# Kernel tuning notes

Measured on AMD Instinct MI355X. Metric: run time of the kernel, lower is better.

## Reference

```python
import jax, jax.numpy as jnp
import numpy as np

REL_CONTEXT = 0.2  # default forward arg

def setup_inputs() -> dict:
    key = jax.random.key(0)
    ks = jax.random.split(key, 8)
    B, M, D = 4096, 2, 2048
    return {
        "x": jax.random.normal(ks[0], (B, M, D), jnp.float32),
        "sub_type_ids": jax.random.randint(ks[1], (B, M), 0, M),
        "modal_weights": jnp.ones((M,), jnp.float32),
        "emb_table": jax.random.normal(ks[2], (M, D), jnp.float32),
        "Wt": jax.random.normal(ks[3], (D, D), jnp.float32) * (1.0 / np.sqrt(D)),
        "bt": jax.random.normal(ks[4], (D,), jnp.float32) * 0.01,
        "Wrc": jax.random.normal(ks[5], (1, D), jnp.float32) * (1.0 / np.sqrt(D)),
        "brc": jax.random.normal(ks[6], (1,), jnp.float32) * 0.01,
    }

def reference(x, sub_type_ids, modal_weights, emb_table, Wt, bt, Wrc, brc):
    B = x.shape[0]
    D = emb_table.shape[1]
    x = x.reshape(B, -1, D)  # [B, M, D]
    # relational gate: Linear(D->1) on a constant vector filled with 0.2 -> scalar
    rc = jnp.full((D,), REL_CONTEXT, dtype=x.dtype)
    zeta = jax.nn.sigmoid(rc @ Wrc.T + brc)  # [1]
    sub = emb_table[sub_type_ids]  # [B, M, D] embedding lookup
    # fused: per-modality Linear + ReLU (replaces the B*M python loop)
    t = jax.nn.relu(jnp.einsum('bmd,ed->bme', x + sub, Wt) + bt)  # [B, M, D]
    h = modal_weights[None, :, None] * t * zeta[0]
    # dropout is identity in eval mode; final ReLU as in the original
    return jax.nn.relu(h)
```

## Files before the change

### kernel.cpp

```cpp
#include <hip/hip_runtime.h>
#include <hip/hip_bf16.h>
#include <math.h>

#define MROWS 8192
#define KDIM  2048
#define NDIM  2048

#define BM 256
#define BN 256
#define BK 64
#define NT (KDIM / BK)

typedef short  v8s __attribute__((ext_vector_type(8)));
typedef float  v4f __attribute__((ext_vector_type(4)));

#define A_OFF   0ull
#define W_OFF   ((unsigned long long)MROWS * KDIM * 2ull)
#define MWZ_OFF (W_OFF + (unsigned long long)NDIM * KDIM * 2ull)

__device__ inline unsigned short f2bf(float f) {
    __hip_bfloat16 h = __float2bfloat16(f);
    return *reinterpret_cast<unsigned short*>(&h);
}

__global__ __launch_bounds__(256) void prep_kernel(
    const float* __restrict__ x, const int* __restrict__ ids,
    const float* __restrict__ mw, const float* __restrict__ emb,
    const float* __restrict__ Wrc, const float* __restrict__ brc,
    const float* __restrict__ Wt,
    unsigned short* __restrict__ Abf, unsigned short* __restrict__ Wbf,
    float* __restrict__ mwz)
{
    const int tid = threadIdx.x;

    if (blockIdx.x == 0) {
        __shared__ float red[256];
        float s = 0.f;
        for (int d = tid; d < KDIM; d += 256) s += Wrc[d];
        red[tid] = s;
        __syncthreads();
        for (int off = 128; off > 0; off >>= 1) {
            if (tid < off) red[tid] += red[tid + off];
            __syncthreads();
        }
        if (tid == 0) {
            float zeta = 1.0f / (1.0f + expf(-(0.2f * red[0] + brc[0])));
            mwz[0] = mw[0] * zeta;
            mwz[1] = mw[1] * zeta;
        }
    }

    const int groupsA = MROWS * KDIM / 8;
    for (int g = blockIdx.x * 256 + tid; g < groupsA; g += gridDim.x * 256) {
        const int row = g >> 8;
        const int off = (g & 255) << 3;
        const int st  = ids[row];
        const float4* xp = (const float4*)(x   + (size_t)row * KDIM + off);
        const float4* ep = (const float4*)(emb + (size_t)st  * KDIM + off);
        float4 x0 = xp[0], x1 = xp[1];
        float4 e0 = ep[0], e1 = ep[1];
        v8s o;
        o[0] = (short)f2bf(x0.x + e0.x);
        o[1] = (short)f2bf(x0.y + e0.y);
        o[2] = (short)f2bf(x0.z + e0.z);
        o[3] = (short)f2bf(x0.w + e0.w);
        o[4] = (short)f2bf(x1.x + e1.x);
        o[5] = (short)f2bf(x1.y + e1.y);
        o[6] = (short)f2bf(x1.z + e1.z);
        o[7] = (short)f2bf(x1.w + e1.w);
        *(v8s*)(Abf + (size_t)g * 8) = o;
    }

    const int groupsW = NDIM * KDIM / 8;
    for (int g = blockIdx.x * 256 + tid; g < groupsW; g += gridDim.x * 256) {
        const float4* wp = (const float4*)(Wt + (size_t)g * 8);
        float4 w0 = wp[0], w1 = wp[1];
        v8s o;
        o[0] = (short)f2bf(w0.x); o[1] = (short)f2bf(w0.y);
        o[2] = (short)f2bf(w0.z); o[3] = (short)f2bf(w0.w);
        o[4] = (short)f2bf(w1.x); o[5] = (short)f2bf(w1.y);
        o[6] = (short)f2bf(w1.z); o[7] = (short)f2bf(w1.w);
        *(v8s*)(Wbf + (size_t)g * 8) = o;
    }
}


#define SBAR()   __builtin_amdgcn_s_barrier()
#define LGKM0()  asm volatile("s_waitcnt lgkmcnt(0)" ::: "memory")
#define VMCNT(n) asm volatile("s_waitcnt vmcnt(" #n ")" ::: "memory")

template<int P>
__device__ __forceinline__ void mfma_phase(v4f (&acc)[8][4],
                                           const v8s (&b)[4][2],
                                           const v8s (&a)[2][2])
{
    __builtin_amdgcn_s_setprio(1);
    #pragma unroll
    for (int j = 0; j < 4; ++j) {
        acc[2*P  ][j] = __builtin_amdgcn_mfma_f32_16x16x32_bf16(b[j][0], a[0][0], acc[2*P  ][j], 0, 0, 0);
        acc[2*P+1][j] = __builtin_amdgcn_mfma_f32_16x16x32_bf16(b[j][0], a[1][0], acc[2*P+1][j], 0, 0, 0);
    }
    #pragma unroll
    for (int j = 0; j < 4; ++j) {
        acc[2*P  ][j] = __builtin_amdgcn_mfma_f32_16x16x32_bf16(b[j][1], a[0][1], acc[2*P  ][j], 0, 0, 0);
        acc[2*P+1][j] = __builtin_amdgcn_mfma_f32_16x16x32_bf16(b[j][1], a[1][1], acc[2*P+1][j], 0, 0, 0);
    }
    __builtin_amdgcn_s_setprio(0);
}

#define KTILE2(CA, CB, NA, NB, T)                                         \
  {                                                                       \
    if ((T) + 1 < NT) {                                                   \
      stage(NB, gB, (T) + 1, 0); stage(NB, gB, (T) + 1, 1);               \
      stage(NB, gB, (T) + 1, 2); stage(NB, gB, (T) + 1, 3);               \
      stage(NA, gA, (T) + 1, 0); stage(NA, gA, (T) + 1, 1);               \
      stage(NA, gA, (T) + 1, 2); stage(NA, gA, (T) + 1, 3);               \
    }                                                                     \
    v8s a[2][2], b[4][2];                                                 \
    b[0][0] = rdB(CB, 0, 0); b[0][1] = rdB(CB, 0, 1);                     \
    b[1][0] = rdB(CB, 1, 0); b[1][1] = rdB(CB, 1, 1);                     \
    b[2][0] = rdB(CB, 2, 0); b[2][1] = rdB(CB, 2, 1);                     \
    b[3][0] = rdB(CB, 3, 0); b[3][1] = rdB(CB, 3, 1);                     \
    a[0][0] = rdA(CA, 0, 0); a[0][1] = rdA(CA, 0, 1);                     \
    a[1][0] = rdA(CA, 1, 0); a[1][1] = rdA(CA, 1, 1);                     \
    mfma_phase<0>(acc, b, a);                                             \
    a[0][0] = rdA(CA, 2, 0); a[0][1] = rdA(CA, 2, 1);                     \
    a[1][0] = rdA(CA, 3, 0); a[1][1] = rdA(CA, 3, 1);                     \
    mfma_phase<1>(acc, b, a);                                             \
    a[0][0] = rdA(CA, 4, 0); a[0][1] = rdA(CA, 4, 1);                     \
    a[1][0] = rdA(CA, 5, 0); a[1][1] = rdA(CA, 5, 1);                     \
    mfma_phase<2>(acc, b, a);                                             \
    a[0][0] = rdA(CA, 6, 0); a[0][1] = rdA(CA, 6, 1);                     \
    a[1][0] = rdA(CA, 7, 0); a[1][1] = rdA(CA, 7, 1);                     \
    mfma_phase<3>(acc, b, a);                                             \
    LGKM0(); VMCNT(0); SBAR();                                            \
  }

__global__ __launch_bounds__(512, 2) void gemm_kernel(
    const unsigned short* __restrict__ Abf,
    const unsigned short* __restrict__ Wbf,
    const float* __restrict__ bt,
    const float* __restrict__ mwz,
    float* __restrict__ out)
{
    __shared__ __align__(16) unsigned short lA0[BM * BK];
    __shared__ __align__(16) unsigned short lA1[BM * BK];
    __shared__ __align__(16) unsigned short lB0[BN * BK];
    __shared__ __align__(16) unsigned short lB1[BN * BK];

    const int tid  = threadIdx.x;
    const int lane = tid & 63;
    const int wave = tid >> 6;
    const int wr   = wave & 1;
    const int wc   = wave >> 1;
    const int quad = lane >> 4;
    const int mcol = lane & 15;

    const int br = blockIdx.x;
    const int bc = blockIdx.y;

    const unsigned short* gA = Abf + (size_t)(br * BM) * KDIM;
    const unsigned short* gB = Wbf + (size_t)(bc * BN) * KDIM;

    v4f acc[8][4];
    const v4f vzero = {0.f, 0.f, 0.f, 0.f};
    #pragma unroll
    for (int i = 0; i < 8; i++)
        #pragma unroll
        for (int j = 0; j < 4; j++) acc[i][j] = vzero;

    auto stage = [&](unsigned short* dst, const unsigned short* gsrc,
                     int t, int s) {
        const int f   = (s << 9) + tid;
        const int row = f >> 3;
        const int ch  = (f & 7) ^ (row & 7);
        const unsigned short* g = gsrc + (size_t)row * KDIM + ((t & 31) << 6) + (ch << 3);
        __builtin_amdgcn_global_load_lds(
            (const __attribute__((address_space(1))) void*)g,
            (__attribute__((address_space(3))) void*)(dst + ((size_t)f << 3)),
            16, 0, 0);
    };

    auto rdA = [&](const unsigned short* l, int i, int ks) -> v8s {
        const int row = (wr << 7) + (i << 4) + mcol;
        const int c   = ((ks << 2) + quad) ^ (row & 7);
        return *(const v8s*)(l + (row << 6) + (c << 3));
    };
    auto rdB = [&](const unsigned short* l, int j, int ks) -> v8s {
        const int col = (wc << 6) + (j << 4) + mcol;
        const int c   = ((ks << 2) + quad) ^ (col & 7);
        return *(const v8s*)(l + (col << 6) + (c << 3));
    };

    stage(lB0, gB, 0, 0); stage(lB0, gB, 0, 1);
    stage(lB0, gB, 0, 2); stage(lB0, gB, 0, 3);
    stage(lA0, gA, 0, 0); stage(lA0, gA, 0, 1);
    stage(lA0, gA, 0, 2); stage(lA0, gA, 0, 3);
    VMCNT(0);
    SBAR();

    #pragma unroll 1
    for (int tt = 0; tt < NT; tt += 2) {
        KTILE2(lA0, lB0, lA1, lB1, tt);
        KTILE2(lA1, lB1, lA0, lB0, tt + 1);
    }

    const float mz = mwz[mcol & 1];
    #pragma unroll
    for (int j = 0; j < 4; ++j) {
        const int ncol = bc * BN + wc * 64 + j * 16 + quad * 4;
        const float4 b4 = *(const float4*)(bt + ncol);
        #pragma unroll
        for (int i = 0; i < 8; ++i) {
            const int row = br * BM + wr * 128 + i * 16 + mcol;
            float4 o;
            o.x = fmaxf(mz * fmaxf(acc[i][j][0] + b4.x, 0.0f), 0.0f);
            o.y = fmaxf(mz * fmaxf(acc[i][j][1] + b4.y, 0.0f), 0.0f);
            o.z = fmaxf(mz * fmaxf(acc[i][j][2] + b4.z, 0.0f), 0.0f);
            o.w = fmaxf(mz * fmaxf(acc[i][j][3] + b4.w, 0.0f), 0.0f);
            *(float4*)(out + (size_t)row * NDIM + ncol) = o;
        }
    }
}

extern "C" void kernel_launch(void* const* d_in, const int* in_sizes, int n_in,
                              void* d_out, int out_size, void* d_ws, size_t ws_size,
                              hipStream_t stream) {
    const float* x    = (const float*)d_in[0];
    const int*   ids  = (const int*)  d_in[1];
    const float* mw   = (const float*)d_in[2];
    const float* emb  = (const float*)d_in[3];
    const float* Wt   = (const float*)d_in[4];
    const float* bt   = (const float*)d_in[5];
    const float* Wrc  = (const float*)d_in[6];
    const float* brc  = (const float*)d_in[7];
    float* out = (float*)d_out;

    char* ws = (char*)d_ws;
    unsigned short* Abf = (unsigned short*)(ws + A_OFF);
    unsigned short* Wbf = (unsigned short*)(ws + W_OFF);
    float* mwz          = (float*)(ws + MWZ_OFF);

    prep_kernel<<<2048, 256, 0, stream>>>(x, ids, mw, emb, Wrc, brc, Wt,
                                          Abf, Wbf, mwz);

    dim3 grid(MROWS / BM, NDIM / BN);
    gemm_kernel<<<grid, 512, 0, stream>>>(Abf, Wbf, bt, mwz, out);
}
```

Measured before the change: 203.3 us.

## Load W tile directly into registers instead of staging through LDS

Removes the LDS buffers for the B (weight) operand. Each wave now loads its 64-column slice of W straight from global memory into double-buffered registers, prefetching the next k-tile while computing the current one. This halves LDS usage and removes the LDS write and read traffic for B. In exchange, waves that share columns now load the same W data redundantly from global memory/L2, and register pressure rises. The last iteration also loads a wrapped tile (t&31) that is never used, since the bounds guard was removed.

```diff
diff --git a/kernel.cpp b/kernel.cpp
--- a/kernel.cpp
+++ b/kernel.cpp
@@ -108,31 +108,24 @@
     __builtin_amdgcn_s_setprio(0);
 }
 
-#define KTILE2(CA, CB, NA, NB, T)                                         \
+#define KTILE2(CA, NA, BCUR, BNXT, T)                                     \
   {                                                                       \
-    if ((T) + 1 < NT) {                                                   \
-      stage(NB, gB, (T) + 1, 0); stage(NB, gB, (T) + 1, 1);               \
-      stage(NB, gB, (T) + 1, 2); stage(NB, gB, (T) + 1, 3);               \
-      stage(NA, gA, (T) + 1, 0); stage(NA, gA, (T) + 1, 1);               \
-      stage(NA, gA, (T) + 1, 2); stage(NA, gA, (T) + 1, 3);               \
-    }                                                                     \
-    v8s a[2][2], b[4][2];                                                 \
-    b[0][0] = rdB(CB, 0, 0); b[0][1] = rdB(CB, 0, 1);                     \
-    b[1][0] = rdB(CB, 1, 0); b[1][1] = rdB(CB, 1, 1);                     \
-    b[2][0] = rdB(CB, 2, 0); b[2][1] = rdB(CB, 2, 1);                     \
-    b[3][0] = rdB(CB, 3, 0); b[3][1] = rdB(CB, 3, 1);                     \
+    stage(NA, gA, (T) + 1, 0); stage(NA, gA, (T) + 1, 1);                 \
+    stage(NA, gA, (T) + 1, 2); stage(NA, gA, (T) + 1, 3);                 \
+    loadB(BNXT, (T) + 1);                                                 \
+    v8s a[2][2];                                                          \
     a[0][0] = rdA(CA, 0, 0); a[0][1] = rdA(CA, 0, 1);                     \
     a[1][0] = rdA(CA, 1, 0); a[1][1] = rdA(CA, 1, 1);                     \
-    mfma_phase<0>(acc, b, a);                                             \
+    mfma_phase<0>(acc, BCUR, a);                                          \
     a[0][0] = rdA(CA, 2, 0); a[0][1] = rdA(CA, 2, 1);                     \
     a[1][0] = rdA(CA, 3, 0); a[1][1] = rdA(CA, 3, 1);                     \
-    mfma_phase<1>(acc, b, a);                                             \
+    mfma_phase<1>(acc, BCUR, a);                                          \
     a[0][0] = rdA(CA, 4, 0); a[0][1] = rdA(CA, 4, 1);                     \
     a[1][0] = rdA(CA, 5, 0); a[1][1] = rdA(CA, 5, 1);                     \
-    mfma_phase<2>(acc, b, a);                                             \
+    mfma_phase<2>(acc, BCUR, a);                                          \
     a[0][0] = rdA(CA, 6, 0); a[0][1] = rdA(CA, 6, 1);                     \
     a[1][0] = rdA(CA, 7, 0); a[1][1] = rdA(CA, 7, 1);                     \
-    mfma_phase<3>(acc, b, a);                                             \
+    mfma_phase<3>(acc, BCUR, a);                                          \
     LGKM0(); VMCNT(0); SBAR();                                            \
   }
 
@@ -145,8 +138,6 @@
 {
     __shared__ __align__(16) unsigned short lA0[BM * BK];
     __shared__ __align__(16) unsigned short lA1[BM * BK];
-    __shared__ __align__(16) unsigned short lB0[BN * BK];
-    __shared__ __align__(16) unsigned short lB1[BN * BK];
 
     const int tid  = threadIdx.x;
     const int lane = tid & 63;
@@ -160,7 +151,8 @@
     const int bc = blockIdx.y;
 
     const unsigned short* gA = Abf + (size_t)(br * BM) * KDIM;
-    const unsigned short* gB = Wbf + (size_t)(bc * BN) * KDIM;
+    const unsigned short* gBrow =
+        Wbf + (size_t)(bc * BN + wc * 64 + mcol) * KDIM;
 
     v4f acc[8][4];
     const v4f vzero = {0.f, 0.f, 0.f, 0.f};
@@ -181,28 +173,35 @@
             16, 0, 0);
     };
 
+    auto loadB = [&](v8s (&bf)[4][2], int t) {
+        const int kt = (t & 31) << 6;
+        #pragma unroll
+        for (int j = 0; j < 4; ++j) {
+            const unsigned short* p = gBrow + (size_t)(j * 16) * KDIM + kt
+                                    + (quad << 3);
+            bf[j][0] = *(const v8s*)(p);
+            bf[j][1] = *(const v8s*)(p + 32);
+        }
+    };
+
     auto rdA = [&](const unsigned short* l, int i, int ks) -> v8s {
         const int row = (wr << 7) + (i << 4) + mcol;
         const int c   = ((ks << 2) + quad) ^ (row & 7);
         return *(const v8s*)(l + (row << 6) + (c << 3));
     };
-    auto rdB = [&](const unsigned short* l, int j, int ks) -> v8s {
-        const int col = (wc << 6) + (j << 4) + mcol;
-        const int c   = ((ks << 2) + quad) ^ (col & 7);
-        return *(const v8s*)(l + (col << 6) + (c << 3));
-    };
-
-    stage(lB0, gB, 0, 0); stage(lB0, gB, 0, 1);
-    stage(lB0, gB, 0, 2); stage(lB0, gB, 0, 3);
+
+    v8s b0[4][2], b1[4][2];
+
     stage(lA0, gA, 0, 0); stage(lA0, gA, 0, 1);
     stage(lA0, gA, 0, 2); stage(lA0, gA, 0, 3);
+    loadB(b0, 0);
     VMCNT(0);
     SBAR();
 
     #pragma unroll 1
     for (int tt = 0; tt < NT; tt += 2) {
-        KTILE2(lA0, lB0, lA1, lB1, tt);
-        KTILE2(lA1, lB1, lA0, lB0, tt + 1);
+        KTILE2(lA0, lA1, b0, b1, tt);
+        KTILE2(lA1, lA0, b1, b0, tt + 1);
     }
 
     const float mz = mwz[mcol & 1];
```

Measured after the change: 236.6 us. 16.4% more time.
